# Kernel tuning notes

Hardware: AMD Instinct MI355X
Metric: run time of the kernel (lower is better)

## Reference

```python
import jax, jax.numpy as jnp
from jax import lax
import numpy as np


def setup_inputs() -> dict:
    key = jax.random.key(0)
    kx, kw = jax.random.split(key)
    # Binary {0,1} activations: the module's int8-cast/XOR/AND trick is only
    # meaningful XNOR-popcount math for binary inputs.
    x = jax.random.randint(kx, (32, 256, 58, 58), 0, 2).astype(jnp.float32)
    weight = jax.random.normal(kw, (256, 256, 3, 3), dtype=jnp.float32)
    return {"x": x, "weight": weight}


def reference(x, weight):
    # XNORConv2d.forward, stride=1, padding=0 (forward never pads).
    B, C, H, W = x.shape
    O, _, kh, kw = weight.shape
    n = C * H * W  # note: alpha normalizes by INPUT size, as in the source
    N = kh * kw

    # alpha = sum_{c,kh,kw} |w| / n, one scalar per output filter  -> (O,)
    alpha = jnp.sum(jnp.abs(weight), axis=(1, 2, 3)) / n

    # Binarized weights: sign(w) >= 0 -> {0,1}
    bw = (weight >= 0).astype(x.dtype)

    dn = lax.conv_dimension_numbers(x.shape, weight.shape, ("NCHW", "OIHW", "NCHW"))
    conv = lambda a, f: lax.conv_general_dilated(
        a, f, window_strides=(1, 1), padding="VALID", dimension_numbers=dn
    )

    # XNOR match count per (b, o, y, x): S = #(p==f) over c,kh,kw
    #   = conv(p, f) + conv(1-p, 1-f)
    S = conv(x, bw) + conv(1.0 - x, 1.0 - bw)  # (B, O, H', W')

    # popcount per channel = 2*s_c - N; summed over channels -> 2*S - C*N
    res = 2.0 * S - jnp.asarray(C * N, dtype=x.dtype)

    return alpha[None, :, None, None] * res
```

## Files before the change

### kernel.cpp

```cpp
#include <hip/hip_runtime.h>
#include <stdint.h>


#define BATCH 32
#define C_IN 256
#define OCH 256
#define HIN 58
#define WIN2 58
#define HOUT 56
#define WOUT 56
#define TAPS 9
#define WWORDS 8
#define HWIN (HIN * WIN2)
#define HWOUT (HOUT * WOUT)
#define NPOS (BATCH * HWIN)
#define OGRP 32

__global__ __launch_bounds__(256) void pack_x_kernel(
    const float* __restrict__ x, uint32_t* __restrict__ xp)
{
    int t = blockIdx.x * 256 + threadIdx.x;
    int w = t / (NPOS / 2);
    int q = t - w * (NPOS / 2);
    int p = 2 * q;
    int b = p / HWIN;
    int r = p - b * HWIN;
    const float* xb = x + ((size_t)(b * C_IN + w * 32)) * HWIN + r;
    uint32_t m0 = 0u, m1 = 0u;
    #pragma unroll
    for (int j = 0; j < 32; ++j) {
        float2 v = *(const float2*)(xb + (size_t)j * HWIN);
        m0 |= (v.x > 0.5f ? 1u : 0u) << j;
        m1 |= (v.y > 0.5f ? 1u : 0u) << j;
    }
    xp[(size_t)p * WWORDS + w] = m0;
    xp[(size_t)(p + 1) * WWORDS + w] = m1;
}

__global__ __launch_bounds__(256) void pack_w_kernel(
    const float* __restrict__ wt, uint32_t* __restrict__ wq,
    float* __restrict__ sA, float* __restrict__ sB)
{
    int o = blockIdx.x;
    int c = threadIdx.x;
    const float* wb = wt + ((size_t)o * C_IN + c) * TAPS;
    float wv[TAPS];
    float s = 0.f;
    #pragma unroll
    for (int t = 0; t < TAPS; ++t) {
        wv[t] = wb[t];
        s += fabsf(wv[t]);
    }
    int wave = c >> 6, lane = c & 63;
    #pragma unroll
    for (int t = 0; t < TAPS; ++t) {
        unsigned long long m = __ballot(wv[t] >= 0.0f);
        if (lane == 0) {
            wq[((size_t)t * OCH + o) * WWORDS + wave * 2]     = (uint32_t)m;
            wq[((size_t)t * OCH + o) * WWORDS + wave * 2 + 1] = (uint32_t)(m >> 32);
        }
    }
    __shared__ float red[256];
    red[c] = s;
    __syncthreads();
    for (int off = 128; off > 0; off >>= 1) {
        if (c < off) red[c] += red[c + off];
        __syncthreads();
    }
    if (c == 0) {
        float alpha = red[0] / (float)(C_IN * HWIN);
        sA[o] = -2.0f * alpha;
        sB[o] = (float)(C_IN * TAPS) * alpha;
    }
}

__global__ __launch_bounds__(256, 4) void xnor_main_kernel(
    const uint32_t* __restrict__ xp, const uint32_t* __restrict__ wq,
    const float* __restrict__ sA, const float* __restrict__ sB,
    float* __restrict__ out)
{
    __shared__ uint32_t wlds[TAPS * OGRP * WWORDS];

    int obase = blockIdx.y * OGRP;
    #pragma unroll
    for (int i = 0; i < 9; ++i) {
        int L = threadIdx.x + i * 256;
        int tap = L >> 8;
        int oo  = (L >> 3) & (OGRP - 1);
        int k   = L & 7;
        wlds[L] = wq[(((size_t)tap * OCH) + obase + oo) * WWORDS + k];
    }
    __syncthreads();

    int m = blockIdx.x * 256 + threadIdx.x;
    int b = m / HWOUT;
    int r = m - b * HWOUT;
    int oy = r / WOUT;
    int ox = r - oy * WOUT;

    uint32_t acc[OGRP / 2];
    #pragma unroll
    for (int i = 0; i < OGRP / 2; ++i) acc[i] = 0u;

    #pragma unroll 1
    for (int tap = 0; tap < TAPS; ++tap) {
        int dy = tap / 3, dx = tap - dy * 3;
        const uint4* src = (const uint4*)(xp +
            (((size_t)b * HIN + (oy + dy)) * WIN2 + (ox + dx)) * WWORDS);
        uint4 x0 = src[0];
        uint4 x1 = src[1];
        const uint4* wl = (const uint4*)&wlds[tap * OGRP * WWORDS];
        #pragma unroll
        for (int oo = 0; oo < OGRP; oo += 2) {
            uint4 wa = wl[oo * 2 + 0];
            uint4 wb2 = wl[oo * 2 + 1];
            uint4 wc = wl[oo * 2 + 2];
            uint4 wd = wl[oo * 2 + 3];
            uint32_t q0 = __popc(wa.x ^ x0.x) + __popc(wa.y ^ x0.y)
                        + __popc(wa.z ^ x0.z) + __popc(wa.w ^ x0.w);
            uint32_t q1 = __popc(wb2.x ^ x1.x) + __popc(wb2.y ^ x1.y)
                        + __popc(wb2.z ^ x1.z) + __popc(wb2.w ^ x1.w);
            uint32_t q2 = __popc(wc.x ^ x0.x) + __popc(wc.y ^ x0.y)
                        + __popc(wc.z ^ x0.z) + __popc(wc.w ^ x0.w);
            uint32_t q3 = __popc(wd.x ^ x1.x) + __popc(wd.y ^ x1.y)
                        + __popc(wd.z ^ x1.z) + __popc(wd.w ^ x1.w);
            acc[oo >> 1] += (q0 + q1) + ((q2 + q3) << 16);
        }
    }

    size_t ob = ((size_t)b * OCH + obase) * HWOUT + (size_t)oy * WOUT + ox;
    #pragma unroll
    for (int oo = 0; oo < OGRP; oo += 2) {
        uint32_t a = acc[oo >> 1];
        float P0 = (float)(a & 0xFFFFu);
        float P1 = (float)(a >> 16);
        int o0 = obase + oo;
        out[ob + (size_t)oo * HWOUT]       = fmaf(sA[o0],     P0, sB[o0]);
        out[ob + (size_t)(oo + 1) * HWOUT] = fmaf(sA[o0 + 1], P1, sB[o0 + 1]);
    }
}

extern "C" void kernel_launch(void* const* d_in, const int* in_sizes, int n_in,
                              void* d_out, int out_size, void* d_ws, size_t ws_size,
                              hipStream_t stream)
{
    const float* x  = (const float*)d_in[0];
    const float* wt = (const float*)d_in[1];
    float* out = (float*)d_out;

    char* ws = (char*)d_ws;
    uint32_t* xp = (uint32_t*)ws;
    uint32_t* wq = (uint32_t*)(ws + 3444736);
    float*    sA = (float*)(ws + 3444736 + 73728);
    float*    sB = (float*)(ws + 3444736 + 73728 + 1024);

    pack_x_kernel<<<dim3(1682), dim3(256), 0, stream>>>(x, xp);

    pack_w_kernel<<<dim3(OCH), dim3(256), 0, stream>>>(wt, wq, sA, sB);

    xnor_main_kernel<<<dim3(392, 8), dim3(256), 0, stream>>>(xp, wq, sA, sB, out);
}
```

Measured before the change: 317.8 us.

## Retile XNOR kernel to 4 positions per thread and 8 output channels per block

Each thread now computes 4 output positions for 8 output channels instead of 1 position for 32 channels, so every LDS weight read is reused across four positions and the grid becomes 98x32. The intent is to cut LDS traffic per popcount and shrink the per-block weight tile. The cost is that the packed activations are now reloaded from global memory four times as often across the channel groups, and register pressure rises from holding 8 uint4 activation vectors per tap.

```diff
diff --git a/kernel.cpp b/kernel.cpp
--- a/kernel.cpp
+++ b/kernel.cpp
@@ -14,7 +14,8 @@
 #define HWIN (HIN * WIN2)
 #define HWOUT (HOUT * WOUT)
 #define NPOS (BATCH * HWIN)
-#define OGRP 32
+#define OGRP 8
+#define POSP 4
 
 __global__ __launch_bounds__(256) void pack_x_kernel(
     const float* __restrict__ x, uint32_t* __restrict__ xp)
@@ -82,61 +83,90 @@
     __shared__ uint32_t wlds[TAPS * OGRP * WWORDS];
 
     int obase = blockIdx.y * OGRP;
-    #pragma unroll
-    for (int i = 0; i < 9; ++i) {
-        int L = threadIdx.x + i * 256;
-        int tap = L >> 8;
-        int oo  = (L >> 3) & (OGRP - 1);
-        int k   = L & 7;
-        wlds[L] = wq[(((size_t)tap * OCH) + obase + oo) * WWORDS + k];
+    int t = threadIdx.x;
+    if (t < 192) {
+        #pragma unroll
+        for (int i = 0; i < 3; ++i) {
+            int L = t * 3 + i;
+            int tap = L >> 6;
+            int oo  = (L >> 3) & (OGRP - 1);
+            int k   = L & 7;
+            wlds[L] = wq[(((size_t)tap * OCH) + obase + oo) * WWORDS + k];
+        }
     }
     __syncthreads();
 
-    int m = blockIdx.x * 256 + threadIdx.x;
-    int b = m / HWOUT;
-    int r = m - b * HWOUT;
-    int oy = r / WOUT;
-    int ox = r - oy * WOUT;
+    const uint32_t* xbase[POSP];
+    size_t oaddr[POSP];
+    #pragma unroll
+    for (int i = 0; i < POSP; ++i) {
+        int m = blockIdx.x * 1024 + t + i * 256;
+        int b = m / HWOUT;
+        int r = m - b * HWOUT;
+        int oy = r / WOUT;
+        int ox = r - oy * WOUT;
+        xbase[i] = xp + (((size_t)b * HIN + oy) * WIN2 + ox) * WWORDS;
+        oaddr[i] = ((size_t)b * OCH + obase) * HWOUT + (size_t)oy * WOUT + ox;
+    }
 
-    uint32_t acc[OGRP / 2];
+    uint32_t acc[(OGRP / 2) * POSP];
     #pragma unroll
-    for (int i = 0; i < OGRP / 2; ++i) acc[i] = 0u;
+    for (int i = 0; i < (OGRP / 2) * POSP; ++i) acc[i] = 0u;
 
     #pragma unroll 1
     for (int tap = 0; tap < TAPS; ++tap) {
         int dy = tap / 3, dx = tap - dy * 3;
-        const uint4* src = (const uint4*)(xp +
-            (((size_t)b * HIN + (oy + dy)) * WIN2 + (ox + dx)) * WWORDS);
-        uint4 x0 = src[0];
-        uint4 x1 = src[1];
+        int toff = (dy * WIN2 + dx) * WWORDS;
+        uint4 x0[POSP], x1[POSP];
+        #pragma unroll
+        for (int i = 0; i < POSP; ++i) {
+            const uint4* s = (const uint4*)(xbase[i] + toff);
+            x0[i] = s[0];
+            x1[i] = s[1];
+        }
         const uint4* wl = (const uint4*)&wlds[tap * OGRP * WWORDS];
         #pragma unroll
-        for (int oo = 0; oo < OGRP; oo += 2) {
-            uint4 wa = wl[oo * 2 + 0];
-            uint4 wb2 = wl[oo * 2 + 1];
-            uint4 wc = wl[oo * 2 + 2];
-            uint4 wd = wl[oo * 2 + 3];
-            uint32_t q0 = __popc(wa.x ^ x0.x) + __popc(wa.y ^ x0.y)
-                        + __popc(wa.z ^ x0.z) + __popc(wa.w ^ x0.w);
-            uint32_t q1 = __popc(wb2.x ^ x1.x) + __popc(wb2.y ^ x1.y)
-                        + __popc(wb2.z ^ x1.z) + __popc(wb2.w ^ x1.w);
-            uint32_t q2 = __popc(wc.x ^ x0.x) + __popc(wc.y ^ x0.y)
-                        + __popc(wc.z ^ x0.z) + __popc(wc.w ^ x0.w);
-            uint32_t q3 = __popc(wd.x ^ x1.x) + __popc(wd.y ^ x1.y)
-                        + __popc(wd.z ^ x1.z) + __popc(wd.w ^ x1.w);
-            acc[oo >> 1] += (q0 + q1) + ((q2 + q3) << 16);
+        for (int pp = 0; pp < OGRP / 2; ++pp) {
+            uint4 wa = wl[pp * 4 + 0];
+            uint4 wb2 = wl[pp * 4 + 1];
+            uint4 wc = wl[pp * 4 + 2];
+            uint4 wd = wl[pp * 4 + 3];
+            #pragma unroll
+            for (int i = 0; i < POSP; ++i) {
+                uint32_t q0 = __popc(wa.x ^ x0[i].x);
+                q0 += __popc(wa.y ^ x0[i].y);
+                q0 += __popc(wa.z ^ x0[i].z);
+                q0 += __popc(wa.w ^ x0[i].w);
+                q0 += __popc(wb2.x ^ x1[i].x);
+                q0 += __popc(wb2.y ^ x1[i].y);
+                q0 += __popc(wb2.z ^ x1[i].z);
+                q0 += __popc(wb2.w ^ x1[i].w);
+                uint32_t q1 = __popc(wc.x ^ x0[i].x);
+                q1 += __popc(wc.y ^ x0[i].y);
+                q1 += __popc(wc.z ^ x0[i].z);
+                q1 += __popc(wc.w ^ x0[i].w);
+                q1 += __popc(wd.x ^ x1[i].x);
+                q1 += __popc(wd.y ^ x1[i].y);
+                q1 += __popc(wd.z ^ x1[i].z);
+                q1 += __popc(wd.w ^ x1[i].w);
+                acc[pp * POSP + i] += q0 + (q1 << 16);
+            }
         }
     }
 
-    size_t ob = ((size_t)b * OCH + obase) * HWOUT + (size_t)oy * WOUT + ox;
     #pragma unroll
-    for (int oo = 0; oo < OGRP; oo += 2) {
-        uint32_t a = acc[oo >> 1];
-        float P0 = (float)(a & 0xFFFFu);
-        float P1 = (float)(a >> 16);
-        int o0 = obase + oo;
-        out[ob + (size_t)oo * HWOUT]       = fmaf(sA[o0],     P0, sB[o0]);
-        out[ob + (size_t)(oo + 1) * HWOUT] = fmaf(sA[o0 + 1], P1, sB[o0 + 1]);
+    for (int pp = 0; pp < OGRP / 2; ++pp) {
+        int o0 = obase + 2 * pp;
+        float a0 = sA[o0], b0 = sB[o0];
+        float a1 = sA[o0 + 1], b1 = sB[o0 + 1];
+        #pragma unroll
+        for (int i = 0; i < POSP; ++i) {
+            uint32_t a = acc[pp * POSP + i];
+            float P0 = (float)(a & 0xFFFFu);
+            float P1 = (float)(a >> 16);
+            out[oaddr[i] + (size_t)(2 * pp) * HWOUT]     = fmaf(a0, P0, b0);
+            out[oaddr[i] + (size_t)(2 * pp + 1) * HWOUT] = fmaf(a1, P1, b1);
+        }
     }
 }
 
@@ -158,5 +188,5 @@
 
     pack_w_kernel<<<dim3(OCH), dim3(256), 0, stream>>>(wt, wq, sA, sB);
 
-    xnor_main_kernel<<<dim3(392, 8), dim3(256), 0, stream>>>(xp, wq, sA, sB, out);
+    xnor_main_kernel<<<dim3(98, 32), dim3(256), 0, stream>>>(xp, wq, sA, sB, out);
 }
```

New measurement: 322.6 us. Within noise of the previous version (+1.5%).
